# Performance work log

Measured on AMD Instinct MI355X. Metric: run time of the kernel, lower is better.

Reference implementation:

```python
import jax, jax.numpy as jnp
import numpy as np

B, OBS, H, A, E = 131072, 194, 64, 5, 3  # batch, obs dim, hidden, max_action_dim, n event types


def setup_inputs() -> dict:
    key = jax.random.key(0)
    ks = jax.random.split(key, 16)
    s = lambda k, shape, std=0.1: (jax.random.normal(k, shape, dtype=jnp.float32) * std)
    return {
        "x": jax.random.normal(ks[0], (B, OBS), dtype=jnp.float32),
        "action": jax.random.randint(ks[1], (B,), 0, A),
        "W1": s(ks[2], (OBS, H)), "b1": jnp.zeros((H,), jnp.float32),
        "W2": s(ks[3], (H, H)),   "b2": jnp.zeros((H,), jnp.float32),
        "Wh": s(ks[4], (E, H, A), 0.01), "bh": jnp.zeros((E, A), jnp.float32),
        "Wc1": s(ks[5], (OBS, H)), "bc1": jnp.zeros((H,), jnp.float32),
        "Wc2": s(ks[6], (H, H)),   "bc2": jnp.zeros((H,), jnp.float32),
        "Wc3": s(ks[7], (H, 1)),   "bc3": jnp.zeros((1,), jnp.float32),
    }


def reference(x, action, W1, b1, W2, b2, Wh, bh, Wc1, bc1, Wc2, bc2, Wc3, bc3):
    # shared trunk
    feat = jnp.tanh(jnp.tanh(x @ W1 + b1) @ W2 + b2)          # [B, H]
    # route each sample to one of E heads via argmax of first 3 obs dims
    ev = jnp.argmax(x[:, :E], axis=1)                          # [B] int
    all_logits = jnp.einsum('bh,eha->bea', feat, Wh) + bh      # [B, E, A]
    logits = jnp.take_along_axis(
        all_logits, jnp.broadcast_to(ev[:, None, None], (x.shape[0], 1, A)), axis=1
    )[:, 0]                                                    # [B, A]
    logp_all = jax.nn.log_softmax(logits, axis=-1)             # [B, A]
    logp = jnp.take_along_axis(logp_all, action[:, None], axis=1)[:, 0]  # [B]
    entropy = -jnp.sum(jnp.exp(logp_all) * logp_all, axis=-1)  # [B]
    # critic
    value = jnp.tanh(jnp.tanh(x @ Wc1 + bc1) @ Wc2 + bc2) @ Wc3 + bc3    # [B, 1]
    return action, logp, entropy, value
```

## Files before the change

### kernel.cpp

```cpp
#include <hip/hip_runtime.h>
#include <hip/hip_bf16.h>

constexpr int Bt    = 131072;
constexpr int OBS   = 194;
constexpr int NT    = 512;
constexpr int RPB   = 512;
constexpr int ITERS = 4;
constexpr int RS    = 72;
constexpr int LS    = 18;

constexpr int W1B_S  = 0;
constexpr int WC1B_S = 14336;
constexpr int W2B_S  = 28672;
constexpr int WC2B_S = 36864;
constexpr int WHB_S  = 45056;

constexpr int L_W1  = 0;
constexpr int L_WC1 = 28672;
constexpr int L_W2  = 57344;
constexpr int L_WC2 = 73728;
constexpr int L_WH  = 90112;
constexpr int L_HA  = 92160;
constexpr int L_LG  = 129024;
constexpr int L_VB  = 133632;
constexpr int L_TOT = 134144;

typedef short bf8   __attribute__((ext_vector_type(8)));
typedef float f32x4 __attribute__((ext_vector_type(4)));
typedef unsigned int u32;

__device__ __forceinline__ short f2bs(float f) {
    union { __hip_bfloat16 h; short s; } u;
    u.h = __float2bfloat16(f);
    return u.s;
}
__device__ __forceinline__ float bs2f(short s) {
    union { short s; __hip_bfloat16 h; } u;
    u.s = s;
    return __bfloat162float(u.h);
}
__device__ __forceinline__ u32 pk2(float a, float b) {
    union { __hip_bfloat162 h; u32 u; } r;
    r.h = __float22bfloat162_rn(float2{a, b});
    return r.u;
}
__device__ __forceinline__ float fast_tanh(float v) {
    v = fminf(fmaxf(v, -15.f), 15.f);
    float e = __expf(2.f * v);
    return (e - 1.f) * __builtin_amdgcn_rcpf(e + 1.f);
}
__device__ __forceinline__ void dma16(const void* g, void* s) {
    __builtin_amdgcn_global_load_lds(
        (const __attribute__((address_space(1))) u32*)g,
        (__attribute__((address_space(3))) u32*)s, 16, 0, 0);
}

__global__ void __launch_bounds__(256) prep(
    const float* __restrict__ W1, const float* __restrict__ b1,
    const float* __restrict__ W2, const float* __restrict__ Wh,
    const float* __restrict__ Wc1, const float* __restrict__ bc1,
    const float* __restrict__ Wc2, const float* __restrict__ Wc3,
    short* __restrict__ ws)
{
    const int gid = blockIdx.x * 256 + threadIdx.x;
    const int gsz = gridDim.x * 256;

    for (int i = gid; i < 14336; i += gsz) {
        int j = i & 7, l = (i >> 3) & 63, nt = (i >> 9) & 3, kb = i >> 11;
        int k = kb * 32 + ((l >> 4) << 3) + j;
        int n = nt * 16 + (l & 15);
        short v1 = 0, v2 = 0;
        if (k < OBS) {
            v1 = f2bs(W1[k * 64 + n]);
            v2 = f2bs(Wc1[k * 64 + n]);
        } else if (k == OBS) {
            v1 = f2bs(b1[n]);
            v2 = f2bs(bc1[n]);
        }
        ws[W1B_S + i]  = v1;
        ws[WC1B_S + i] = v2;
    }
    for (int i = gid; i < 8192; i += gsz) {
        int j = i & 7, l = (i >> 3) & 63, nt = (i >> 9) & 3, kb = i >> 11;
        int s = kb * 32 + ((l >> 4) << 3) + j;
        int kp = (s & 3) * 16 + (s >> 2);
        int n = nt * 16 + (l & 15);
        ws[W2B_S + i]  = f2bs(W2[kp * 64 + n]);
        ws[WC2B_S + i] = f2bs(Wc2[kp * 64 + n]);
    }
    for (int i = gid; i < 1024; i += gsz) {
        int j = i & 7, l = (i >> 3) & 63, kb = i >> 9;
        int s = kb * 32 + ((l >> 4) << 3) + j;
        int kp = (s & 3) * 16 + (s >> 2);
        int cc = l & 15;
        float v;
        if (cc == 15) v = Wc3[kp];
        else { int e = cc / 5, a = cc - 5 * e; v = Wh[(e * 64 + kp) * 5 + a]; }
        ws[WHB_S + i] = f2bs(v);
    }
}

__global__ void __launch_bounds__(NT, 2) fused_ac(
    const float* __restrict__ x, const int* __restrict__ act_in,
    const float* __restrict__ b2, const float* __restrict__ bc2,
    const float* __restrict__ bh, const float* __restrict__ bc3,
    const short* __restrict__ ws,
    float* __restrict__ out)
{
    __shared__ __align__(16) char smem[L_TOT];

    const int t    = threadIdx.x;
    const int w    = t >> 6;
    const int l    = t & 63;
    const int q    = l >> 4;
    const int c    = l & 15;
    const int base = blockIdx.x * RPB;

    #pragma unroll
    for (int i = 0; i < 12; ++i) {
        int idx = i * NT + t;
        if (idx < 5760)
            dma16(((const char*)ws) + idx * 16, smem + idx * 16);
    }

    float b2v[4], bc2v[4];
    #pragma unroll
    for (int nt = 0; nt < 4; ++nt) {
        b2v[nt]  = b2[nt * 16 + c];
        bc2v[nt] = bc2[nt * 16 + c];
    }
    float bhv = (c < 15) ? bh[c] : bc3[0];

    float2 raw[24]; float2 rt6;
    auto loadraw = [&](int gm2) {
        const float* xr = x + (size_t)gm2 * OBS;
        #pragma unroll
        for (int kb = 0; kb < 6; ++kb) {
            const float2* p = reinterpret_cast<const float2*>(xr + kb * 32 + q * 8);
            raw[kb * 4 + 0] = p[0]; raw[kb * 4 + 1] = p[1];
            raw[kb * 4 + 2] = p[2]; raw[kb * 4 + 3] = p[3];
        }
        rt6 = float2{0.f, 0.f};
        if (q == 0) rt6 = *reinterpret_cast<const float2*>(xr + 192);
    };
    union AF { u32 u[4]; bf8 v; } af[7];
    int ev = 0;
    auto packaf = [&]() {
        #pragma unroll
        for (int kb = 0; kb < 6; ++kb) {
            af[kb].u[0] = pk2(raw[kb * 4 + 0].x, raw[kb * 4 + 0].y);
            af[kb].u[1] = pk2(raw[kb * 4 + 1].x, raw[kb * 4 + 1].y);
            af[kb].u[2] = pk2(raw[kb * 4 + 2].x, raw[kb * 4 + 2].y);
            af[kb].u[3] = pk2(raw[kb * 4 + 3].x, raw[kb * 4 + 3].y);
        }
        af[6].u[0] = 0; af[6].u[1] = 0; af[6].u[2] = 0; af[6].u[3] = 0;
        if (q == 0) {
            af[6].u[0] = pk2(rt6.x, rt6.y);
            af[6].u[1] = pk2(1.0f, 0.0f);
        }
        ev = 0;
        float bbest = raw[0].x;
        if (raw[0].y > bbest) { bbest = raw[0].y; ev = 1; }
        if (raw[1].x > bbest) { ev = 2; }
    };

    loadraw(base + w * 16 + c);

    __syncthreads();

    packaf();

    const bf8* fW1L  = reinterpret_cast<const bf8*>(smem + L_W1);
    const bf8* fWc1L = reinterpret_cast<const bf8*>(smem + L_WC1);
    const bf8* fW2L  = reinterpret_cast<const bf8*>(smem + L_W2);
    const bf8* fWc2L = reinterpret_cast<const bf8*>(smem + L_WC2);
    const bf8* fWhL  = reinterpret_cast<const bf8*>(smem + L_WH);
    short* ha = reinterpret_cast<short*>(smem + L_HA + w * 4608);
    short* hc = ha + 2304 / 2;
    short* lw = reinterpret_cast<short*>(smem + L_LG + w * 576);
    float* vb = reinterpret_cast<float*>(smem + L_VB + w * 64);

    #pragma unroll 1
    for (int i = 0; i < ITERS; ++i) {
        const int gm = base + i * 128 + w * 16 + c;
        int act = 0;
        if (l < 16) act = act_in[gm];
        const int evc = ev;

        if (i + 1 < ITERS) loadraw(base + (i + 1) * 128 + w * 16 + c);

        f32x4 aa[4], ac[4];
        #pragma unroll
        for (int nt = 0; nt < 4; ++nt) {
            aa[nt] = f32x4{0.f, 0.f, 0.f, 0.f};
            ac[nt] = f32x4{0.f, 0.f, 0.f, 0.f};
        }
        #pragma unroll
        for (int kb = 0; kb < 7; ++kb) {
            bf8 a = af[kb].v;
            #pragma unroll
            for (int nt = 0; nt < 4; ++nt) {
                aa[nt] = __builtin_amdgcn_mfma_f32_16x16x32_bf16(a, fW1L [(kb * 4 + nt) * 64 + l], aa[nt], 0, 0, 0);
                ac[nt] = __builtin_amdgcn_mfma_f32_16x16x32_bf16(a, fWc1L[(kb * 4 + nt) * 64 + l], ac[nt], 0, 0, 0);
            }
        }
        #pragma unroll
        for (int r = 0; r < 4; ++r) {
            uint2 pa, pc;
            pa.x = pk2(fast_tanh(aa[0][r]), fast_tanh(aa[1][r]));
            pa.y = pk2(fast_tanh(aa[2][r]), fast_tanh(aa[3][r]));
            pc.x = pk2(fast_tanh(ac[0][r]), fast_tanh(ac[1][r]));
            pc.y = pk2(fast_tanh(ac[2][r]), fast_tanh(ac[3][r]));
            *reinterpret_cast<uint2*>(&ha[(q * 4 + r) * RS + 4 * c]) = pa;
            *reinterpret_cast<uint2*>(&hc[(q * 4 + r) * RS + 4 * c]) = pc;
        }

        #pragma unroll
        for (int nt = 0; nt < 4; ++nt) {
            aa[nt] = f32x4{b2v[nt], b2v[nt], b2v[nt], b2v[nt]};
            ac[nt] = f32x4{bc2v[nt], bc2v[nt], bc2v[nt], bc2v[nt]};
        }
        #pragma unroll
        for (int kb = 0; kb < 2; ++kb) {
            bf8 xa = *reinterpret_cast<const bf8*>(&ha[c * RS + kb * 32 + q * 8]);
            bf8 xc = *reinterpret_cast<const bf8*>(&hc[c * RS + kb * 32 + q * 8]);
            #pragma unroll
            for (int nt = 0; nt < 4; ++nt) {
                aa[nt] = __builtin_amdgcn_mfma_f32_16x16x32_bf16(xa, fW2L [(kb * 4 + nt) * 64 + l], aa[nt], 0, 0, 0);
                ac[nt] = __builtin_amdgcn_mfma_f32_16x16x32_bf16(xc, fWc2L[(kb * 4 + nt) * 64 + l], ac[nt], 0, 0, 0);
            }
        }
        #pragma unroll
        for (int r = 0; r < 4; ++r) {
            uint2 pa, pc;
            pa.x = pk2(fast_tanh(aa[0][r]), fast_tanh(aa[1][r]));
            pa.y = pk2(fast_tanh(aa[2][r]), fast_tanh(aa[3][r]));
            pc.x = pk2(fast_tanh(ac[0][r]), fast_tanh(ac[1][r]));
            pc.y = pk2(fast_tanh(ac[2][r]), fast_tanh(ac[3][r]));
            *reinterpret_cast<uint2*>(&ha[(q * 4 + r) * RS + 4 * c]) = pa;
            *reinterpret_cast<uint2*>(&hc[(q * 4 + r) * RS + 4 * c]) = pc;
        }

        {
            f32x4 lg = f32x4{bhv, bhv, bhv, bhv};
            f32x4 vv = f32x4{bhv, bhv, bhv, bhv};
            #pragma unroll
            for (int kb = 0; kb < 2; ++kb) {
                bf8 bw = fWhL[kb * 64 + l];
                bf8 fa = *reinterpret_cast<const bf8*>(&ha[c * RS + kb * 32 + q * 8]);
                bf8 fc = *reinterpret_cast<const bf8*>(&hc[c * RS + kb * 32 + q * 8]);
                lg = __builtin_amdgcn_mfma_f32_16x16x32_bf16(fa, bw, lg, 0, 0, 0);
                vv = __builtin_amdgcn_mfma_f32_16x16x32_bf16(fc, bw, vv, 0, 0, 0);
            }
            #pragma unroll
            for (int r = 0; r < 4; ++r)
                lw[(q * 4 + r) * LS + c] = f2bs(lg[r]);
            if (c == 15) {
                #pragma unroll
                for (int r = 0; r < 4; ++r)
                    vb[q * 4 + r] = vv[r];
            }
        }

        if (l < 16) {
            float lg[5];
            #pragma unroll
            for (int a = 0; a < 5; ++a)
                lg[a] = bs2f(lw[c * LS + evc * 5 + a]);
            float mx = lg[0];
            #pragma unroll
            for (int a = 1; a < 5; ++a) mx = fmaxf(mx, lg[a]);
            float se = 0.f;
            #pragma unroll
            for (int a = 0; a < 5; ++a) se += __expf(lg[a] - mx);
            float lse = __logf(se) + mx;
            float lsel = lg[0];
            #pragma unroll
            for (int a = 1; a < 5; ++a) lsel = (act == a) ? lg[a] : lsel;
            float ent = 0.f;
            #pragma unroll
            for (int a = 0; a < 5; ++a) { float lp = lg[a] - lse; ent -= __expf(lp) * lp; }

            out[gm]          = (float)act;
            out[Bt + gm]     = lsel - lse;
            out[2 * Bt + gm] = ent;
            out[3 * Bt + gm] = vb[c];
        }

        if (i + 1 < ITERS) packaf();
    }
}

extern "C" void kernel_launch(void* const* d_in, const int* in_sizes, int n_in,
                              void* d_out, int out_size, void* d_ws, size_t ws_size,
                              hipStream_t stream) {
    const float* x   = (const float*)d_in[0];
    const int*   act = (const int*)  d_in[1];
    const float* W1  = (const float*)d_in[2];
    const float* b1  = (const float*)d_in[3];
    const float* W2  = (const float*)d_in[4];
    const float* b2  = (const float*)d_in[5];
    const float* Wh  = (const float*)d_in[6];
    const float* bh  = (const float*)d_in[7];
    const float* Wc1 = (const float*)d_in[8];
    const float* bc1 = (const float*)d_in[9];
    const float* Wc2 = (const float*)d_in[10];
    const float* bc2 = (const float*)d_in[11];
    const float* Wc3 = (const float*)d_in[12];
    const float* bc3 = (const float*)d_in[13];
    float* out = (float*)d_out;
    short* ws  = (short*)d_ws;

    hipLaunchKernelGGL(prep, dim3(32), dim3(256), 0, stream,
                       W1, b1, W2, Wh, Wc1, bc1, Wc2, Wc3, ws);
    hipLaunchKernelGGL(fused_ac, dim3(Bt / RPB), dim3(NT), 0, stream,
                       x, act, b2, bc2, bh, bc3, ws, out);
}
```

Measured before the change: 183.1 us.

## Split actor and critic into separate block roles to halve LDS and raise occupancy

```diff
diff --git a/kernel.cpp b/kernel.cpp
--- a/kernel.cpp
+++ b/kernel.cpp
@@ -4,26 +4,18 @@
 constexpr int Bt    = 131072;
 constexpr int OBS   = 194;
 constexpr int NT    = 512;
-constexpr int RPB   = 512;
 constexpr int ITERS = 4;
 constexpr int RS    = 72;
 constexpr int LS    = 18;
 
-constexpr int W1B_S  = 0;
-constexpr int WC1B_S = 14336;
-constexpr int W2B_S  = 28672;
-constexpr int WC2B_S = 36864;
-constexpr int WHB_S  = 45056;
-
-constexpr int L_W1  = 0;
-constexpr int L_WC1 = 28672;
-constexpr int L_W2  = 57344;
-constexpr int L_WC2 = 73728;
-constexpr int L_WH  = 90112;
-constexpr int L_HA  = 92160;
-constexpr int L_LG  = 129024;
-constexpr int L_VB  = 133632;
-constexpr int L_TOT = 134144;
+constexpr int ROLE_S = 23552;
+
+constexpr int L_W1f = 0;
+constexpr int L_W2f = 28672;
+constexpr int L_WHf = 45056;
+constexpr int L_H   = 47104;
+constexpr int L_AUX = 65536;
+constexpr int L_TOT = 70144;
 
 typedef short bf8   __attribute__((ext_vector_type(8)));
 typedef float f32x4 __attribute__((ext_vector_type(4)));
@@ -77,16 +69,16 @@
             v1 = f2bs(b1[n]);
             v2 = f2bs(bc1[n]);
         }
-        ws[W1B_S + i]  = v1;
-        ws[WC1B_S + i] = v2;
+        ws[i]          = v1;
+        ws[ROLE_S + i] = v2;
     }
     for (int i = gid; i < 8192; i += gsz) {
         int j = i & 7, l = (i >> 3) & 63, nt = (i >> 9) & 3, kb = i >> 11;
         int s = kb * 32 + ((l >> 4) << 3) + j;
         int kp = (s & 3) * 16 + (s >> 2);
         int n = nt * 16 + (l & 15);
-        ws[W2B_S + i]  = f2bs(W2[kp * 64 + n]);
-        ws[WC2B_S + i] = f2bs(Wc2[kp * 64 + n]);
+        ws[14336 + i]          = f2bs(W2[kp * 64 + n]);
+        ws[ROLE_S + 14336 + i] = f2bs(Wc2[kp * 64 + n]);
     }
     for (int i = gid; i < 1024; i += gsz) {
         int j = i & 7, l = (i >> 3) & 63, kb = i >> 9;
@@ -96,11 +88,13 @@
         float v;
         if (cc == 15) v = Wc3[kp];
         else { int e = cc / 5, a = cc - 5 * e; v = Wh[(e * 64 + kp) * 5 + a]; }
-        ws[WHB_S + i] = f2bs(v);
-    }
-}
-
-__global__ void __launch_bounds__(NT, 2) fused_ac(
+        short vs = f2bs(v);
+        ws[22528 + i]          = vs;
+        ws[ROLE_S + 22528 + i] = vs;
+    }
+}
+
+__global__ void __launch_bounds__(NT, 4) fused_ac(
     const float* __restrict__ x, const int* __restrict__ act_in,
     const float* __restrict__ b2, const float* __restrict__ bc2,
     const float* __restrict__ bh, const float* __restrict__ bc3,
@@ -114,38 +108,56 @@
     const int l    = t & 63;
     const int q    = l >> 4;
     const int c    = l & 15;
-    const int base = blockIdx.x * RPB;
-
+    const int b    = blockIdx.x;
+    const int g    = b >> 4;
+    const int role = (b >> 3) & 1;
+    const int sub  = b & 7;
+    const int base = g * 4096 + sub * 512;
+
+    {
+        const char* gsrc = ((const char*)ws) + (size_t)role * 47104;
+        #pragma unroll
+        for (int i = 0; i < 6; ++i) {
+            int idx = i * NT + t;
+            if (idx < 2944)
+                dma16(gsrc + idx * 16, smem + idx * 16);
+        }
+    }
+
+    const float* bL2 = role ? bc2 : b2;
+    float b2v[4];
     #pragma unroll
-    for (int i = 0; i < 12; ++i) {
-        int idx = i * NT + t;
-        if (idx < 5760)
-            dma16(((const char*)ws) + idx * 16, smem + idx * 16);
-    }
-
-    float b2v[4], bc2v[4];
-    #pragma unroll
-    for (int nt = 0; nt < 4; ++nt) {
-        b2v[nt]  = b2[nt * 16 + c];
-        bc2v[nt] = bc2[nt * 16 + c];
-    }
-    float bhv = (c < 15) ? bh[c] : bc3[0];
-
-    float2 raw[24]; float2 rt6;
-    auto loadraw = [&](int gm2) {
-        const float* xr = x + (size_t)gm2 * OBS;
-        #pragma unroll
-        for (int kb = 0; kb < 6; ++kb) {
-            const float2* p = reinterpret_cast<const float2*>(xr + kb * 32 + q * 8);
-            raw[kb * 4 + 0] = p[0]; raw[kb * 4 + 1] = p[1];
-            raw[kb * 4 + 2] = p[2]; raw[kb * 4 + 3] = p[3];
-        }
-        rt6 = float2{0.f, 0.f};
-        if (q == 0) rt6 = *reinterpret_cast<const float2*>(xr + 192);
-    };
-    union AF { u32 u[4]; bf8 v; } af[7];
-    int ev = 0;
-    auto packaf = [&]() {
+    for (int nt = 0; nt < 4; ++nt) b2v[nt] = bL2[nt * 16 + c];
+    float bhv = role ? bc3[0] : ((c < 15) ? bh[c] : 0.f);
+
+    __syncthreads();
+
+    const bf8* fL1 = reinterpret_cast<const bf8*>(smem + L_W1f);
+    const bf8* fL2 = reinterpret_cast<const bf8*>(smem + L_W2f);
+    const bf8* fWh = reinterpret_cast<const bf8*>(smem + L_WHf);
+    short* hb = reinterpret_cast<short*>(smem + L_H + w * 2304);
+    short* lw = reinterpret_cast<short*>(smem + L_AUX + w * 576);
+    float* vb = reinterpret_cast<float*>(smem + L_AUX + w * 576);
+
+    #pragma unroll 1
+    for (int i = 0; i < ITERS; ++i) {
+        const int gm = base + i * 128 + w * 16 + c;
+
+        float2 raw[24]; float2 rt6 = float2{0.f, 0.f};
+        {
+            const float* xr = x + (size_t)gm * OBS;
+            #pragma unroll
+            for (int kb = 0; kb < 6; ++kb) {
+                const float2* p = reinterpret_cast<const float2*>(xr + kb * 32 + q * 8);
+                raw[kb * 4 + 0] = p[0]; raw[kb * 4 + 1] = p[1];
+                raw[kb * 4 + 2] = p[2]; raw[kb * 4 + 3] = p[3];
+            }
+            if (q == 0) rt6 = *reinterpret_cast<const float2*>(xr + 192);
+        }
+        int act = 0;
+        if (role == 0 && l < 16) act = act_in[gm];
+
+        union AF { u32 u[4]; bf8 v; } af[7];
         #pragma unroll
         for (int kb = 0; kb < 6; ++kb) {
             af[kb].u[0] = pk2(raw[kb * 4 + 0].x, raw[kb * 4 + 0].y);
@@ -158,136 +170,96 @@
             af[6].u[0] = pk2(rt6.x, rt6.y);
             af[6].u[1] = pk2(1.0f, 0.0f);
         }
-        ev = 0;
-        float bbest = raw[0].x;
-        if (raw[0].y > bbest) { bbest = raw[0].y; ev = 1; }
-        if (raw[1].x > bbest) { ev = 2; }
-    };
-
-    loadraw(base + w * 16 + c);
-
-    __syncthreads();
-
-    packaf();
-
-    const bf8* fW1L  = reinterpret_cast<const bf8*>(smem + L_W1);
-    const bf8* fWc1L = reinterpret_cast<const bf8*>(smem + L_WC1);
-    const bf8* fW2L  = reinterpret_cast<const bf8*>(smem + L_W2);
-    const bf8* fWc2L = reinterpret_cast<const bf8*>(smem + L_WC2);
-    const bf8* fWhL  = reinterpret_cast<const bf8*>(smem + L_WH);
-    short* ha = reinterpret_cast<short*>(smem + L_HA + w * 4608);
-    short* hc = ha + 2304 / 2;
-    short* lw = reinterpret_cast<short*>(smem + L_LG + w * 576);
-    float* vb = reinterpret_cast<float*>(smem + L_VB + w * 64);
-
-    #pragma unroll 1
-    for (int i = 0; i < ITERS; ++i) {
-        const int gm = base + i * 128 + w * 16 + c;
-        int act = 0;
-        if (l < 16) act = act_in[gm];
-        const int evc = ev;
-
-        if (i + 1 < ITERS) loadraw(base + (i + 1) * 128 + w * 16 + c);
-
-        f32x4 aa[4], ac[4];
-        #pragma unroll
-        for (int nt = 0; nt < 4; ++nt) {
-            aa[nt] = f32x4{0.f, 0.f, 0.f, 0.f};
-            ac[nt] = f32x4{0.f, 0.f, 0.f, 0.f};
-        }
+        int ev = 0;
+        {
+            float bbest = raw[0].x;
+            if (raw[0].y > bbest) { bbest = raw[0].y; ev = 1; }
+            if (raw[1].x > bbest) { ev = 2; }
+        }
+
+        f32x4 acc[4];
+        #pragma unroll
+        for (int nt = 0; nt < 4; ++nt) acc[nt] = f32x4{0.f, 0.f, 0.f, 0.f};
         #pragma unroll
         for (int kb = 0; kb < 7; ++kb) {
             bf8 a = af[kb].v;
             #pragma unroll
-            for (int nt = 0; nt < 4; ++nt) {
-                aa[nt] = __builtin_amdgcn_mfma_f32_16x16x32_bf16(a, fW1L [(kb * 4 + nt) * 64 + l], aa[nt], 0, 0, 0);
-                ac[nt] = __builtin_amdgcn_mfma_f32_16x16x32_bf16(a, fWc1L[(kb * 4 + nt) * 64 + l], ac[nt], 0, 0, 0);
-            }
+            for (int nt = 0; nt < 4; ++nt)
+                acc[nt] = __builtin_amdgcn_mfma_f32_16x16x32_bf16(a, fL1[(kb * 4 + nt) * 64 + l], acc[nt], 0, 0, 0);
         }
         #pragma unroll
         for (int r = 0; r < 4; ++r) {
-            uint2 pa, pc;
-            pa.x = pk2(fast_tanh(aa[0][r]), fast_tanh(aa[1][r]));
-            pa.y = pk2(fast_tanh(aa[2][r]), fast_tanh(aa[3][r]));
-            pc.x = pk2(fast_tanh(ac[0][r]), fast_tanh(ac[1][r]));
-            pc.y = pk2(fast_tanh(ac[2][r]), fast_tanh(ac[3][r]));
-            *reinterpret_cast<uint2*>(&ha[(q * 4 + r) * RS + 4 * c]) = pa;
-            *reinterpret_cast<uint2*>(&hc[(q * 4 + r) * RS + 4 * c]) = pc;
-        }
-
-        #pragma unroll
-        for (int nt = 0; nt < 4; ++nt) {
-            aa[nt] = f32x4{b2v[nt], b2v[nt], b2v[nt], b2v[nt]};
-            ac[nt] = f32x4{bc2v[nt], bc2v[nt], bc2v[nt], bc2v[nt]};
-        }
+            uint2 pa;
+            pa.x = pk2(fast_tanh(acc[0][r]), fast_tanh(acc[1][r]));
+            pa.y = pk2(fast_tanh(acc[2][r]), fast_tanh(acc[3][r]));
+            *reinterpret_cast<uint2*>(&hb[(q * 4 + r) * RS + 4 * c]) = pa;
+        }
+
+        #pragma unroll
+        for (int nt = 0; nt < 4; ++nt)
+            acc[nt] = f32x4{b2v[nt], b2v[nt], b2v[nt], b2v[nt]};
         #pragma unroll
         for (int kb = 0; kb < 2; ++kb) {
-            bf8 xa = *reinterpret_cast<const bf8*>(&ha[c * RS + kb * 32 + q * 8]);
-            bf8 xc = *reinterpret_cast<const bf8*>(&hc[c * RS + kb * 32 + q * 8]);
-            #pragma unroll
-            for (int nt = 0; nt < 4; ++nt) {
-                aa[nt] = __builtin_amdgcn_mfma_f32_16x16x32_bf16(xa, fW2L [(kb * 4 + nt) * 64 + l], aa[nt], 0, 0, 0);
-                ac[nt] = __builtin_amdgcn_mfma_f32_16x16x32_bf16(xc, fWc2L[(kb * 4 + nt) * 64 + l], ac[nt], 0, 0, 0);
-            }
+            bf8 xa = *reinterpret_cast<const bf8*>(&hb[c * RS + kb * 32 + q * 8]);
+            #pragma unroll
+            for (int nt = 0; nt < 4; ++nt)
+                acc[nt] = __builtin_amdgcn_mfma_f32_16x16x32_bf16(xa, fL2[(kb * 4 + nt) * 64 + l], acc[nt], 0, 0, 0);
         }
         #pragma unroll
         for (int r = 0; r < 4; ++r) {
-            uint2 pa, pc;
-            pa.x = pk2(fast_tanh(aa[0][r]), fast_tanh(aa[1][r]));
-            pa.y = pk2(fast_tanh(aa[2][r]), fast_tanh(aa[3][r]));
-            pc.x = pk2(fast_tanh(ac[0][r]), fast_tanh(ac[1][r]));
-            pc.y = pk2(fast_tanh(ac[2][r]), fast_tanh(ac[3][r]));
-            *reinterpret_cast<uint2*>(&ha[(q * 4 + r) * RS + 4 * c]) = pa;
-            *reinterpret_cast<uint2*>(&hc[(q * 4 + r) * RS + 4 * c]) = pc;
+            uint2 pa;
+            pa.x = pk2(fast_tanh(acc[0][r]), fast_tanh(acc[1][r]));
+            pa.y = pk2(fast_tanh(acc[2][r]), fast_tanh(acc[3][r]));
+            *reinterpret_cast<uint2*>(&hb[(q * 4 + r) * RS + 4 * c]) = pa;
         }
 
         {
-            f32x4 lg = f32x4{bhv, bhv, bhv, bhv};
-            f32x4 vv = f32x4{bhv, bhv, bhv, bhv};
+            f32x4 hd = f32x4{bhv, bhv, bhv, bhv};
             #pragma unroll
             for (int kb = 0; kb < 2; ++kb) {
-                bf8 bw = fWhL[kb * 64 + l];
-                bf8 fa = *reinterpret_cast<const bf8*>(&ha[c * RS + kb * 32 + q * 8]);
-                bf8 fc = *reinterpret_cast<const bf8*>(&hc[c * RS + kb * 32 + q * 8]);
-                lg = __builtin_amdgcn_mfma_f32_16x16x32_bf16(fa, bw, lg, 0, 0, 0);
-                vv = __builtin_amdgcn_mfma_f32_16x16x32_bf16(fc, bw, vv, 0, 0, 0);
-            }
-            #pragma unroll
-            for (int r = 0; r < 4; ++r)
-                lw[(q * 4 + r) * LS + c] = f2bs(lg[r]);
-            if (c == 15) {
+                bf8 bw = fWh[kb * 64 + l];
+                bf8 fa = *reinterpret_cast<const bf8*>(&hb[c * RS + kb * 32 + q * 8]);
+                hd = __builtin_amdgcn_mfma_f32_16x16x32_bf16(fa, bw, hd, 0, 0, 0);
+            }
+            if (role == 0) {
                 #pragma unroll
                 for (int r = 0; r < 4; ++r)
-                    vb[q * 4 + r] = vv[r];
-            }
-        }
-
-        if (l < 16) {
-            float lg[5];
-            #pragma unroll
-            for (int a = 0; a < 5; ++a)
-                lg[a] = bs2f(lw[c * LS + evc * 5 + a]);
-            float mx = lg[0];
-            #pragma unroll
-            for (int a = 1; a < 5; ++a) mx = fmaxf(mx, lg[a]);
-            float se = 0.f;
-            #pragma unroll
-            for (int a = 0; a < 5; ++a) se += __expf(lg[a] - mx);
-            float lse = __logf(se) + mx;
-            float lsel = lg[0];
-            #pragma unroll
-            for (int a = 1; a < 5; ++a) lsel = (act == a) ? lg[a] : lsel;
-            float ent = 0.f;
-            #pragma unroll
-            for (int a = 0; a < 5; ++a) { float lp = lg[a] - lse; ent -= __expf(lp) * lp; }
-
-            out[gm]          = (float)act;
-            out[Bt + gm]     = lsel - lse;
-            out[2 * Bt + gm] = ent;
-            out[3 * Bt + gm] = vb[c];
-        }
-
-        if (i + 1 < ITERS) packaf();
+                    lw[(q * 4 + r) * LS + c] = f2bs(hd[r]);
+            } else if (c == 15) {
+                #pragma unroll
+                for (int r = 0; r < 4; ++r)
+                    vb[q * 4 + r] = hd[r];
+            }
+        }
+
+        if (role == 0) {
+            if (l < 16) {
+                float lg[5];
+                #pragma unroll
+                for (int a = 0; a < 5; ++a)
+                    lg[a] = bs2f(lw[c * LS + ev * 5 + a]);
+                float mx = lg[0];
+                #pragma unroll
+                for (int a = 1; a < 5; ++a) mx = fmaxf(mx, lg[a]);
+                float se = 0.f;
+                #pragma unroll
+                for (int a = 0; a < 5; ++a) se += __expf(lg[a] - mx);
+                float lse = __logf(se) + mx;
+                float lsel = lg[0];
+                #pragma unroll
+                for (int a = 1; a < 5; ++a) lsel = (act == a) ? lg[a] : lsel;
+                float ent = 0.f;
+                #pragma unroll
+                for (int a = 0; a < 5; ++a) { float lp = lg[a] - lse; ent -= __expf(lp) * lp; }
+
+                out[gm]          = (float)act;
+                out[Bt + gm]     = lsel - lse;
+                out[2 * Bt + gm] = ent;
+            }
+        } else {
+            if (l < 16)
+                out[3 * Bt + gm] = vb[c];
+        }
     }
 }
 
@@ -313,6 +285,6 @@
 
     hipLaunchKernelGGL(prep, dim3(32), dim3(256), 0, stream,
                        W1, b1, W2, Wh, Wc1, bc1, Wc2, Wc3, ws);
-    hipLaunchKernelGGL(fused_ac, dim3(Bt / RPB), dim3(NT), 0, stream,
+    hipLaunchKernelGGL(fused_ac, dim3(512), dim3(NT), 0, stream,
                        x, act, b2, bc2, bh, bc3, ws, out);
 }
```

Measured after the change: 183.2 us. Within noise of the previous version (+0.1%).
